# Performance work log

Hardware: AMD Instinct MI355X
Metric: run time of the kernel (lower is better)

The kernel has to match this reference:

```python
import jax, jax.numpy as jnp
import numpy as np

N_NODES = 50000
N_FEAT = 128
HIDDEN = 3
N_EDGES = 600000
N_POWERS = 3


def setup_inputs() -> dict:
    key = jax.random.key(0)
    ks = jax.random.split(key, 6)
    x = jax.random.normal(ks[0], (N_NODES, N_FEAT), dtype=jnp.float32)
    edge_index = jax.random.randint(ks[1], (N_POWERS, 2, N_EDGES), 0, N_NODES, dtype=jnp.int64)
    # MLP params for the 3 adjacency powers, stacked on the leading axis.
    # torch Linear(in,out) stored transposed here: y = x @ W + b.
    Wa = jax.random.normal(ks[2], (N_POWERS, N_FEAT, HIDDEN), dtype=jnp.float32) * (1.0 / np.sqrt(N_FEAT))
    ba = jax.random.normal(ks[3], (N_POWERS, HIDDEN), dtype=jnp.float32) * 0.01
    Wb = jax.random.normal(ks[4], (N_POWERS, HIDDEN, 1), dtype=jnp.float32) * (1.0 / np.sqrt(HIDDEN))
    bb = jax.random.normal(ks[5], (N_POWERS, 1), dtype=jnp.float32) * 0.01
    return {"x": x, "edge_index": edge_index, "Wa": Wa, "ba": ba, "Wb": Wb, "bb": bb}


def reference(x, edge_index, Wa, ba, Wb, bb):
    # Gather source/target node features per edge, per adjacency power.
    x_j = x[edge_index[:, 0]]          # [P, E, F]
    x_i = x[edge_index[:, 1]]          # [P, E, F]
    abs_dif = jnp.abs(x_j - x_i)       # [P, E, F]
    # Tiny per-edge MLP: Linear -> ReLU -> Linear -> Sigmoid (separate params per power).
    h = jax.nn.relu(jnp.einsum('pef,pfh->peh', abs_dif, Wa) + ba[:, None, :])  # [P, E, H]
    w = jax.nn.sigmoid(jnp.einsum('peh,pho->peo', h, Wb) + bb[:, None, :])     # [P, E, 1]
    return w[..., 0]                   # [P, E] edge weights for each power
```

## Files before the change

### kernel.cpp

```cpp
#include <hip/hip_runtime.h>
#include <math.h>

#define N_NODES 50000
#define N_FEAT  128
#define N_EDGES 600000
#define N_POWERS 3

#define PAIRS 5
#define EDGES_PER_BLK (64 * PAIRS)

#define NB64 64
#define CAP64 10240
#define CHUNK 2048
#define NCHUNK 293

typedef _Float16 half2v __attribute__((ext_vector_type(2)));
typedef unsigned u32x4  __attribute__((ext_vector_type(4)));
union HU { unsigned u; half2v h; };

__device__ __forceinline__ int bj_of(int j) { return j / 6250; }

__global__ __launch_bounds__(256) void conv_x_plain(const float* __restrict__ x,
                                                    unsigned* __restrict__ xh,
                                                    const float* __restrict__ Wa,
                                                    unsigned* __restrict__ wah,
                                                    int* __restrict__ cur) {
    const int t = blockIdx.x * 256 + threadIdx.x;
    const float4* x4 = (const float4*)x;
    float4 a = x4[(size_t)t * 2];
    float4 b = x4[(size_t)t * 2 + 1];
    HU p0, p1, p2, p3;
    p0.h = half2v{(_Float16)a.x, (_Float16)a.y};
    p1.h = half2v{(_Float16)a.z, (_Float16)a.w};
    p2.h = half2v{(_Float16)b.x, (_Float16)b.y};
    p3.h = half2v{(_Float16)b.z, (_Float16)b.w};
    ((uint4*)xh)[t] = uint4{p0.u, p1.u, p2.u, p3.u};
    if (blockIdx.x == 0 && threadIdx.x < 192) {
        const int tt = threadIdx.x;
        #pragma unroll
        for (int q = 0; q < 3; ++q) {
            int idx = tt + q * 192;
            int c  = idx % 3;
            int pk = idx / 3;
            int k  = pk % 64;
            int p  = pk / 64;
            float w0 = Wa[p * 384 + (2 * k) * 3 + c];
            float w1 = Wa[p * 384 + (2 * k + 1) * 3 + c];
            HU u; u.h = half2v{(_Float16)w0, (_Float16)w1};
            wah[idx] = u.u;
        }
    }
    if (cur != nullptr && blockIdx.x == 1 && threadIdx.x < N_POWERS * NB64)
        cur[threadIdx.x] = 0;
}

__global__ __launch_bounds__(256) void scatter_onepass(const int* __restrict__ edge_index,
                                                       unsigned* __restrict__ su,
                                                       int* __restrict__ inv,
                                                       int* __restrict__ cur) {
    __shared__ int tot[4][NB64];
    __shared__ int sh_w[4][NB64];
    __shared__ int sh_lbase[NB64];
    __shared__ int sh_delta[NB64];
    __shared__ int sh_vt;
    __shared__ unsigned pay[CHUNK];
    __shared__ int dlt[CHUNK];

    const int p = blockIdx.y, chunk = blockIdx.x;
    const int tid  = threadIdx.x;
    const int lane = tid & 63;
    const int wave = tid >> 6;
    const int* ej = edge_index + (size_t)p * 2 * N_EDGES;
    const int* ei = ej + N_EDGES;
    const int base = chunk * CHUNK;

    int jj[8], ii[8], sbk[8], off[8];
    int run = 0;
    #pragma unroll
    for (int k = 0; k < 8; ++k) {
        const int e = base + k * 256 + tid;
        const bool valid = e < N_EDGES;
        jj[k] = __builtin_nontemporal_load(ej + (valid ? e : 0));
        ii[k] = __builtin_nontemporal_load(ei + (valid ? e : 0));
        const int b = bj_of(jj[k]) * 8 + bj_of(ii[k]);
        sbk[k] = b;
        const unsigned long long m0 = __ballot(b & 1);
        const unsigned long long m1 = __ballot(b & 2);
        const unsigned long long m2 = __ballot(b & 4);
        const unsigned long long m3 = __ballot(b & 8);
        const unsigned long long m4 = __ballot(b & 16);
        const unsigned long long m5 = __ballot(b & 32);
        const unsigned long long vm = __ballot(valid);
        unsigned long long m = ((b & 1) ? m0 : ~m0);
        m &= ((b & 2)  ? m1 : ~m1);
        m &= ((b & 4)  ? m2 : ~m2);
        m &= ((b & 8)  ? m3 : ~m3);
        m &= ((b & 16) ? m4 : ~m4);
        m &= ((b & 32) ? m5 : ~m5);
        m &= vm;
        const int rank = (int)__popcll(m & ((1ull << lane) - 1ull));
        unsigned long long mm = ((lane & 1) ? m0 : ~m0);
        mm &= ((lane & 2)  ? m1 : ~m1);
        mm &= ((lane & 4)  ? m2 : ~m2);
        mm &= ((lane & 8)  ? m3 : ~m3);
        mm &= ((lane & 16) ? m4 : ~m4);
        mm &= ((lane & 32) ? m5 : ~m5);
        mm &= vm;
        const int cnt = (int)__popcll(mm);
        const int pre = __shfl(run, b, 64);
        off[k] = pre + rank;
        run += cnt;
    }
    tot[wave][lane] = run;
    __syncthreads();

    if (tid < NB64) {
        const int t0 = tot[0][tid], t1 = tot[1][tid], t2 = tot[2][tid], t3 = tot[3][tid];
        const int bt = t0 + t1 + t2 + t3;
        int s = bt;
        #pragma unroll
        for (int d = 1; d < 64; d <<= 1) {
            int u = __shfl_up(s, d, 64);
            if (tid >= d) s += u;
        }
        const int lb = s - bt;
        const int g  = atomicAdd(&cur[p * NB64 + tid], bt);
        sh_lbase[tid] = lb;
        sh_delta[tid] = (p * NB64 + tid) * CAP64 + g - lb;
        sh_w[0][tid] = 0;
        sh_w[1][tid] = t0;
        sh_w[2][tid] = t0 + t1;
        sh_w[3][tid] = t0 + t1 + t2;
        if (tid == 63) sh_vt = lb + bt;
    }
    __syncthreads();

    #pragma unroll
    for (int k = 0; k < 8; ++k) {
        const int e = base + k * 256 + tid;
        if (e < N_EDGES) {
            const int b = sbk[k];
            const int pos = sh_lbase[b] + sh_w[wave][b] + off[k];
            pay[pos] = (unsigned)(jj[k] | (ii[k] << 16));
            dlt[pos] = sh_delta[b];
            inv[(size_t)p * N_EDGES + e] = sh_delta[b] + pos;
        }
    }
    __syncthreads();

    const int vt = sh_vt;
    #pragma unroll
    for (int k = 0; k < 8; ++k) {
        const int pos = k * 256 + tid;
        if (pos < vt)
            su[(size_t)(dlt[pos] + pos)] = pay[pos];
    }
}

template<int PAT>
__device__ __forceinline__ float swz(float v) {
    return __int_as_float(__builtin_amdgcn_ds_swizzle(__float_as_int(v), PAT));
}

__device__ __forceinline__ void dot3_8(const u32x4& qa0, const u32x4& qa1,
                                       const u32x4& qb0, const u32x4& qb1,
                                       const HU wa[8][3],
                                       float& h0, float& h1, float& h2) {
    unsigned ua[8] = {qa0[0], qa0[1], qa0[2], qa0[3], qa1[0], qa1[1], qa1[2], qa1[3]};
    unsigned ub[8] = {qb0[0], qb0[1], qb0[2], qb0[3], qb1[0], qb1[1], qb1[2], qb1[3]};
    h0 = 0.f; h1 = 0.f; h2 = 0.f;
    #pragma unroll
    for (int k = 0; k < 8; ++k) {
        HU a, b, d;
        a.u = ua[k]; b.u = ub[k];
        d.h = a.h - b.h;
        d.u &= 0x7fff7fffu;
        h0 = __builtin_amdgcn_fdot2(d.h, wa[k][0].h, h0, false);
        h1 = __builtin_amdgcn_fdot2(d.h, wa[k][1].h, h1, false);
        h2 = __builtin_amdgcn_fdot2(d.h, wa[k][2].h, h2, false);
    }
}

__global__ __launch_bounds__(256, 4) void adj_kernel_sorted(
    const unsigned* __restrict__ xh,
    unsigned* su,
    const int* __restrict__ cur,
    const unsigned* __restrict__ wah,
    const float* __restrict__ ba,
    const float* __restrict__ Wb,
    const float* __restrict__ bb)
{
    const int p    = blockIdx.y;
    const int bj   = blockIdx.x & 7;
    const int k    = (blockIdx.x >> 3) & 31;
    const int bi   = blockIdx.x >> 8;
    const int sb   = bj * 8 + bi;
    const int tid  = threadIdx.x;
    const int lane = tid & 63;
    const int wave = tid >> 6;
    const int sub  = lane & 7;
    const int grp  = lane >> 3;

    const int count = cur[p * NB64 + sb];
    const int base  = k * EDGES_PER_BLK;
    if (base >= count) return;

    HU wa[8][3];
    {
        const unsigned* wp = wah + ((size_t)p * 64 + sub * 8) * 3;
        #pragma unroll
        for (int kk = 0; kk < 8; ++kk) {
            wa[kk][0].u = wp[kk * 3 + 0];
            wa[kk][1].u = wp[kk * 3 + 1];
            wa[kk][2].u = wp[kk * 3 + 2];
        }
        #pragma unroll
        for (int kk = 0; kk < 8; ++kk) {
            asm volatile("" : "+v"(wa[kk][0].u), "+v"(wa[kk][1].u), "+v"(wa[kk][2].u));
        }
    }

    const float ba0 = ba[p * 3 + 0], ba1 = ba[p * 3 + 1], ba2 = ba[p * 3 + 2];
    const float wb0 = Wb[p * 3 + 0], wb1 = Wb[p * 3 + 1], wb2 = Wb[p * 3 + 2];
    const float bbp = bb[p];

    unsigned* sup = su + (size_t)(p * NB64 + sb) * CAP64;

    const int eoff = wave * 8 + grp;
    const int roff = sub * 8;
    const int cm1  = count - 1;

    unsigned q[2 * PAIRS];
    #pragma unroll
    for (int it = 0; it < PAIRS; ++it) {
        const int r1 = base + it * 64 + eoff;
        q[2 * it]     = __builtin_nontemporal_load(sup + min(r1, cm1));
        q[2 * it + 1] = __builtin_nontemporal_load(sup + min(r1 + 32, cm1));
    }

    u32x4 A0, A1, B0, B1, C0, C1, D0, D1;
    {
        const int j1 = (int)(q[0] & 0xFFFFu), i1 = (int)(q[0] >> 16);
        const int j2 = (int)(q[1] & 0xFFFFu), i2 = (int)(q[1] >> 16);
        const u32x4* rj1 = (const u32x4*)(xh + ((size_t)j1 << 6) + roff);
        const u32x4* ri1 = (const u32x4*)(xh + ((size_t)i1 << 6) + roff);
        const u32x4* rj2 = (const u32x4*)(xh + ((size_t)j2 << 6) + roff);
        const u32x4* ri2 = (const u32x4*)(xh + ((size_t)i2 << 6) + roff);
        A0 = rj1[0]; A1 = rj1[1]; B0 = ri1[0]; B1 = ri1[1];
        C0 = rj2[0]; C1 = rj2[1]; D0 = ri2[0]; D1 = ri2[1];
    }

    #pragma unroll
    for (int it = 0; it < PAIRS; ++it) {
        u32x4 nA0, nA1, nB0, nB1, nC0, nC1, nD0, nD1;
        if (it + 1 < PAIRS) {
            const int j1 = (int)(q[2 * it + 2] & 0xFFFFu), i1 = (int)(q[2 * it + 2] >> 16);
            const int j2 = (int)(q[2 * it + 3] & 0xFFFFu), i2 = (int)(q[2 * it + 3] >> 16);
            const u32x4* rj1 = (const u32x4*)(xh + ((size_t)j1 << 6) + roff);
            const u32x4* ri1 = (const u32x4*)(xh + ((size_t)i1 << 6) + roff);
            const u32x4* rj2 = (const u32x4*)(xh + ((size_t)j2 << 6) + roff);
            const u32x4* ri2 = (const u32x4*)(xh + ((size_t)i2 << 6) + roff);
            nA0 = rj1[0]; nA1 = rj1[1]; nB0 = ri1[0]; nB1 = ri1[1];
            nC0 = rj2[0]; nC1 = rj2[1]; nD0 = ri2[0]; nD1 = ri2[1];
        }

        float h0a, h1a, h2a, h0b, h1b, h2b;
        dot3_8(A0, A1, B0, B1, wa, h0a, h1a, h2a);
        dot3_8(C0, C1, D0, D1, wa, h0b, h1b, h2b);

        h0a += swz<0x041F>(h0a); h1a += swz<0x041F>(h1a); h2a += swz<0x041F>(h2a);
        h0b += swz<0x041F>(h0b); h1b += swz<0x041F>(h1b); h2b += swz<0x041F>(h2b);
        h0a += swz<0x081F>(h0a); h1a += swz<0x081F>(h1a); h2a += swz<0x081F>(h2a);
        h0b += swz<0x081F>(h0b); h1b += swz<0x081F>(h1b); h2b += swz<0x081F>(h2b);
        h0a += swz<0x101F>(h0a); h1a += swz<0x101F>(h1a); h2a += swz<0x101F>(h2a);
        h0b += swz<0x101F>(h0b); h1b += swz<0x101F>(h1b); h2b += swz<0x101F>(h2b);

        if (sub == 0) {
            const int r1 = base + it * 64 + eoff;
            const int r2 = r1 + 32;
            if (r1 < count) {
                float r0  = fmaxf(h0a + ba0, 0.f);
                float r1f = fmaxf(h1a + ba1, 0.f);
                float r2f = fmaxf(h2a + ba2, 0.f);
                float s   = fmaf(r0, wb0, fmaf(r1f, wb1, fmaf(r2f, wb2, bbp)));
                ((float*)sup)[r1] = 1.f / (1.f + __expf(-s));
            }
            if (r2 < count) {
                float r0  = fmaxf(h0b + ba0, 0.f);
                float r1f = fmaxf(h1b + ba1, 0.f);
                float r2f = fmaxf(h2b + ba2, 0.f);
                float s   = fmaf(r0, wb0, fmaf(r1f, wb1, fmaf(r2f, wb2, bbp)));
                ((float*)sup)[r2] = 1.f / (1.f + __expf(-s));
            }
        }

        if (it + 1 < PAIRS) {
            A0 = nA0; A1 = nA1; B0 = nB0; B1 = nB1;
            C0 = nC0; C1 = nC1; D0 = nD0; D1 = nD1;
        }
    }
}

__global__ __launch_bounds__(256) void unscatter_kernel(const unsigned* __restrict__ su,
                                                        const int* __restrict__ inv,
                                                        float* __restrict__ out) {
    const int p  = blockIdx.y;
    const int t4 = (blockIdx.x * 256 + threadIdx.x) * 4;
    if (t4 >= N_EDGES) return;
    const int4 iv = *(const int4*)(inv + (size_t)p * N_EDGES + t4);
    const float* w = (const float*)su;
    float4 o;
    o.x = w[iv.x]; o.y = w[iv.y]; o.z = w[iv.z]; o.w = w[iv.w];
    __builtin_nontemporal_store(o.x, out + (size_t)p * N_EDGES + t4 + 0);
    __builtin_nontemporal_store(o.y, out + (size_t)p * N_EDGES + t4 + 1);
    __builtin_nontemporal_store(o.z, out + (size_t)p * N_EDGES + t4 + 2);
    __builtin_nontemporal_store(o.w, out + (size_t)p * N_EDGES + t4 + 3);
}

__global__ __launch_bounds__(256) void adj_kernel_f16(
    const unsigned* __restrict__ xh,
    const unsigned* __restrict__ wah,
    const int*   __restrict__ edge_index,
    const float* __restrict__ ba,
    const float* __restrict__ Wb,
    const float* __restrict__ bb,
    float* __restrict__ out)
{
    const int p    = blockIdx.y;
    const int tid  = threadIdx.x;
    const int lane = tid & 63;
    const int wave = tid >> 6;
    const int sub  = lane & 7;
    const int grp  = lane >> 3;

    HU wa[8][3];
    {
        const unsigned* wp = wah + ((size_t)p * 64 + sub * 8) * 3;
        #pragma unroll
        for (int k = 0; k < 8; ++k) {
            wa[k][0].u = wp[k * 3 + 0];
            wa[k][1].u = wp[k * 3 + 1];
            wa[k][2].u = wp[k * 3 + 2];
        }
        #pragma unroll
        for (int k = 0; k < 8; ++k) {
            asm volatile("" : "+v"(wa[k][0].u), "+v"(wa[k][1].u), "+v"(wa[k][2].u));
        }
    }

    const float ba0 = ba[p * 3 + 0], ba1 = ba[p * 3 + 1], ba2 = ba[p * 3 + 2];
    const float wb0 = Wb[p * 3 + 0], wb1 = Wb[p * 3 + 1], wb2 = Wb[p * 3 + 2];
    const float bbp = bb[p];

    const int* ej = edge_index + (size_t)p * 2 * N_EDGES;
    const int* ei = ej + N_EDGES;
    float* outp = out + (size_t)p * N_EDGES;

    const int e_blk = blockIdx.x * EDGES_PER_BLK;
    const int eoff  = wave * 8 + grp;
    const int roff  = sub * 8;

    #pragma unroll
    for (int it = 0; it < PAIRS; ++it) {
        const int e1 = e_blk + it * 64 + eoff;
        const int e2 = e1 + 32;
        const int j1 = __builtin_nontemporal_load(ej + e1);
        const int i1 = __builtin_nontemporal_load(ei + e1);
        const int j2 = __builtin_nontemporal_load(ej + e2);
        const int i2 = __builtin_nontemporal_load(ei + e2);

        const u32x4* rj1 = (const u32x4*)(xh + ((size_t)j1 << 6) + roff);
        const u32x4* ri1 = (const u32x4*)(xh + ((size_t)i1 << 6) + roff);
        const u32x4* rj2 = (const u32x4*)(xh + ((size_t)j2 << 6) + roff);
        const u32x4* ri2 = (const u32x4*)(xh + ((size_t)i2 << 6) + roff);
        u32x4 a0 = rj1[0], a1 = rj1[1];
        u32x4 b0 = ri1[0], b1 = ri1[1];
        u32x4 c0 = rj2[0], c1 = rj2[1];
        u32x4 d0 = ri2[0], d1 = ri2[1];

        float h0a, h1a, h2a, h0b, h1b, h2b;
        dot3_8(a0, a1, b0, b1, wa, h0a, h1a, h2a);
        dot3_8(c0, c1, d0, d1, wa, h0b, h1b, h2b);

        h0a += swz<0x041F>(h0a); h1a += swz<0x041F>(h1a); h2a += swz<0x041F>(h2a);
        h0b += swz<0x041F>(h0b); h1b += swz<0x041F>(h1b); h2b += swz<0x041F>(h2b);
        h0a += swz<0x081F>(h0a); h1a += swz<0x081F>(h1a); h2a += swz<0x081F>(h2a);
        h0b += swz<0x081F>(h0b); h1b += swz<0x081F>(h1b); h2b += swz<0x081F>(h2b);
        h0a += swz<0x101F>(h0a); h1a += swz<0x101F>(h1a); h2a += swz<0x101F>(h2a);
        h0b += swz<0x101F>(h0b); h1b += swz<0x101F>(h1b); h2b += swz<0x101F>(h2b);

        if (sub == 0) {
            float r0 = fmaxf(h0a + ba0, 0.f);
            float r1 = fmaxf(h1a + ba1, 0.f);
            float r2 = fmaxf(h2a + ba2, 0.f);
            float s  = fmaf(r0, wb0, fmaf(r1, wb1, fmaf(r2, wb2, bbp)));
            __builtin_nontemporal_store(1.f / (1.f + __expf(-s)), outp + e1);
            r0 = fmaxf(h0b + ba0, 0.f);
            r1 = fmaxf(h1b + ba1, 0.f);
            r2 = fmaxf(h2b + ba2, 0.f);
            s  = fmaf(r0, wb0, fmaf(r1, wb1, fmaf(r2, wb2, bbp)));
            __builtin_nontemporal_store(1.f / (1.f + __expf(-s)), outp + e2);
        }
    }
}

__global__ __launch_bounds__(256) void adj_kernel_f32(
    const float* __restrict__ x,
    const int*   __restrict__ edge_index,
    const float* __restrict__ Wa,
    const float* __restrict__ ba,
    const float* __restrict__ Wb,
    const float* __restrict__ bb,
    float* __restrict__ out)
{
    const int p    = blockIdx.y;
    const int tid  = threadIdx.x;
    const int lane = tid & 63;
    const int wave = tid >> 6;
    const int sub  = lane & 15;
    const int grp  = lane >> 4;
    const int f0 = sub * 8;

    const float* Wap = Wa + (size_t)p * N_FEAT * 3;
    float wa0[8], wa1[8], wa2[8];
    #pragma unroll
    for (int k = 0; k < 8; ++k) {
        wa0[k] = Wap[(f0 + k) * 3 + 0];
        wa1[k] = Wap[(f0 + k) * 3 + 1];
        wa2[k] = Wap[(f0 + k) * 3 + 2];
    }
    const float ba0 = ba[p * 3 + 0], ba1 = ba[p * 3 + 1], ba2 = ba[p * 3 + 2];
    const float wb0 = Wb[p * 3 + 0], wb1 = Wb[p * 3 + 1], wb2 = Wb[p * 3 + 2];
    const float bbp = bb[p];

    const int e = blockIdx.x * 16 + wave * 4 + grp;
    const int* ej = edge_index + (size_t)p * 2 * N_EDGES;
    const int* ei = ej + N_EDGES;
    const int j = ej[e];
    const int i = ei[e];

    const float4* xj = (const float4*)(x + (size_t)j * N_FEAT + f0);
    const float4* xi = (const float4*)(x + (size_t)i * N_FEAT + f0);
    float4 a0 = xj[0], a1 = xj[1];
    float4 b0 = xi[0], b1 = xi[1];

    float d[8];
    d[0] = fabsf(a0.x - b0.x); d[1] = fabsf(a0.y - b0.y);
    d[2] = fabsf(a0.z - b0.z); d[3] = fabsf(a0.w - b0.w);
    d[4] = fabsf(a1.x - b1.x); d[5] = fabsf(a1.y - b1.y);
    d[6] = fabsf(a1.z - b1.z); d[7] = fabsf(a1.w - b1.w);

    float h0 = 0.f, h1 = 0.f, h2 = 0.f;
    #pragma unroll
    for (int k = 0; k < 8; ++k) {
        h0 = fmaf(d[k], wa0[k], h0);
        h1 = fmaf(d[k], wa1[k], h1);
        h2 = fmaf(d[k], wa2[k], h2);
    }
    #pragma unroll
    for (int m = 1; m < 16; m <<= 1) {
        h0 += __shfl_xor(h0, m, 64);
        h1 += __shfl_xor(h1, m, 64);
        h2 += __shfl_xor(h2, m, 64);
    }
    if (sub == 0) {
        float r0 = fmaxf(h0 + ba0, 0.f);
        float r1 = fmaxf(h1 + ba1, 0.f);
        float r2 = fmaxf(h2 + ba2, 0.f);
        float s  = fmaf(r0, wb0, fmaf(r1, wb1, fmaf(r2, wb2, bbp)));
        float w  = 1.f / (1.f + expf(-s));
        out[(size_t)p * N_EDGES + e] = w;
    }
}

extern "C" void kernel_launch(void* const* d_in, const int* in_sizes, int n_in,
                              void* d_out, int out_size, void* d_ws, size_t ws_size,
                              hipStream_t stream) {
    const float* x          = (const float*)d_in[0];
    const int*   edge_index = (const int*)d_in[1];
    const float* Wa         = (const float*)d_in[2];
    const float* ba         = (const float*)d_in[3];
    const float* Wb         = (const float*)d_in[4];
    const float* bb         = (const float*)d_in[5];
    float* out = (float*)d_out;

    const size_t x_bytes   = (size_t)N_NODES * N_FEAT * 2;
    const size_t su_bytes  = (size_t)N_POWERS * NB64 * CAP64 * 4;
    const size_t inv_bytes = (size_t)N_POWERS * N_EDGES * 4;
    const size_t wa_bytes  = 2304;
    const size_t cur_bytes = N_POWERS * NB64 * 4;
    const size_t need_full = x_bytes + su_bytes + inv_bytes + wa_bytes + cur_bytes;

    if (ws_size >= need_full) {
        char* w = (char*)d_ws;
        unsigned* xh  = (unsigned*)w;
        unsigned* su  = (unsigned*)(w + x_bytes);
        int*      inv = (int*)(w + x_bytes + su_bytes);
        unsigned* wah = (unsigned*)(w + x_bytes + su_bytes + inv_bytes);
        int*      cur = (int*)(w + x_bytes + su_bytes + inv_bytes + wa_bytes);

        conv_x_plain<<<N_NODES * N_FEAT / 2048, 256, 0, stream>>>(x, xh, Wa, wah, cur);
        scatter_onepass<<<dim3(NCHUNK, N_POWERS), 256, 0, stream>>>(edge_index, su, inv, cur);
        dim3 grid(NB64 * (CAP64 / EDGES_PER_BLK), N_POWERS);
        adj_kernel_sorted<<<grid, 256, 0, stream>>>(xh, su, cur, wah, ba, Wb, bb);
        unscatter_kernel<<<dim3((N_EDGES / 4 + 255) / 256, N_POWERS), 256, 0, stream>>>(
            su, inv, out);
    } else if (ws_size >= x_bytes + wa_bytes) {
        unsigned* xh  = (unsigned*)d_ws;
        unsigned* wah = (unsigned*)((char*)d_ws + x_bytes);
        conv_x_plain<<<N_NODES * N_FEAT / 2048, 256, 0, stream>>>(x, xh, Wa, wah, nullptr);
        dim3 grid(N_EDGES / EDGES_PER_BLK, N_POWERS);
        adj_kernel_f16<<<grid, 256, 0, stream>>>(xh, wah, edge_index, ba, Wb, bb, out);
    } else {
        dim3 grid((N_EDGES + 15) / 16, N_POWERS);
        adj_kernel_f32<<<grid, 256, 0, stream>>>(x, edge_index, Wa, ba, Wb, bb, out);
    }
}
```

Measured before the change: 176.8 us.

## Bucket edges by source node range and counting-sort within buckets by source

Edges are now bucketed into 64 bins by source node range only, instead of by a joint source/target 8x8 grid. A new per-bucket counting sort in shared memory orders each bucket by exact source node, and a fixup kernel rewrites the inverse permutation, using the output buffer as scratch for the permutation. Target-row loads become nontemporal while source rows keep normal caching. The aim is cache reuse of source rows, paid for with two extra kernel launches, extra passes over the sorted payload, and the risk of a bucket overflowing CAP64 under uniform counts.

```diff
diff --git a/kernel.cpp b/kernel.cpp
--- a/kernel.cpp
+++ b/kernel.cpp
@@ -10,6 +10,7 @@
 #define EDGES_PER_BLK (64 * PAIRS)
 
 #define NB64 64
+#define NJB 782
 #define CAP64 10240
 #define CHUNK 2048
 #define NCHUNK 293
@@ -17,8 +18,6 @@
 typedef _Float16 half2v __attribute__((ext_vector_type(2)));
 typedef unsigned u32x4  __attribute__((ext_vector_type(4)));
 union HU { unsigned u; half2v h; };
-
-__device__ __forceinline__ int bj_of(int j) { return j / 6250; }
 
 __global__ __launch_bounds__(256) void conv_x_plain(const float* __restrict__ x,
                                                     unsigned* __restrict__ xh,
@@ -82,7 +81,7 @@
         const bool valid = e < N_EDGES;
         jj[k] = __builtin_nontemporal_load(ej + (valid ? e : 0));
         ii[k] = __builtin_nontemporal_load(ei + (valid ? e : 0));
-        const int b = bj_of(jj[k]) * 8 + bj_of(ii[k]);
+        const int b = jj[k] / NJB;
         sbk[k] = b;
         const unsigned long long m0 = __ballot(b & 1);
         const unsigned long long m1 = __ballot(b & 2);
@@ -157,6 +156,93 @@
     }
 }
 
+__global__ __launch_bounds__(256) void sortj_kernel(unsigned* __restrict__ su,
+                                                    int* __restrict__ perm,
+                                                    const int* __restrict__ cur) {
+    __shared__ int hist[NJB];
+    __shared__ unsigned spay[CAP64];
+    __shared__ int wsum[4];
+    __shared__ int csum;
+    const int p = blockIdx.y, b = blockIdx.x;
+    const int tid = threadIdx.x;
+    const int count = cur[p * NB64 + b];
+    const size_t gbase = (size_t)(p * NB64 + b) * CAP64;
+
+    if (tid == 0) {
+        int s = 0;
+        for (int t = 0; t < b; ++t) s += cur[p * NB64 + t];
+        csum = s;
+    }
+    for (int t = tid; t < NJB; t += 256) hist[t] = 0;
+    __syncthreads();
+
+    const int j0 = b * NJB;
+    for (int s = tid; s < count; s += 256) {
+        const unsigned v = su[gbase + s];
+        atomicAdd(&hist[(int)(v & 0xFFFFu) - j0], 1);
+    }
+    __syncthreads();
+
+    int loc[4]; int ts = 0;
+    #pragma unroll
+    for (int q = 0; q < 4; ++q) {
+        const int idx = tid * 4 + q;
+        loc[q] = (idx < NJB) ? hist[idx] : 0;
+        ts += loc[q];
+    }
+    const int lane = tid & 63, wv = tid >> 6;
+    int ps = ts;
+    #pragma unroll
+    for (int d = 1; d < 64; d <<= 1) { int u = __shfl_up(ps, d, 64); if (lane >= d) ps += u; }
+    if (lane == 63) wsum[wv] = ps;
+    __syncthreads();
+    int wbase = 0;
+    #pragma unroll
+    for (int wq = 0; wq < 4; ++wq) wbase += (wq < wv) ? wsum[wq] : 0;
+    int run = wbase + (ps - ts);
+    __syncthreads();
+    #pragma unroll
+    for (int q = 0; q < 4; ++q) {
+        const int idx = tid * 4 + q;
+        if (idx < NJB) hist[idx] = run;
+        run += loc[q];
+    }
+    __syncthreads();
+
+    const int cb = p * N_EDGES + csum;
+    for (int s = tid; s < count; s += 256) {
+        const unsigned v = su[gbase + s];
+        const int np = atomicAdd(&hist[(int)(v & 0xFFFFu) - j0], 1);
+        spay[np] = v;
+        perm[cb + s] = np;
+    }
+    __syncthreads();
+    for (int s = tid; s < count; s += 256)
+        su[gbase + s] = spay[s];
+}
+
+__global__ __launch_bounds__(256) void fixinv_kernel(int* __restrict__ inv,
+                                                     const int* __restrict__ perm,
+                                                     const int* __restrict__ cur) {
+    __shared__ int cbase[N_POWERS * NB64];
+    const int tid = threadIdx.x;
+    if (tid < N_POWERS * NB64) {
+        const int p = tid / NB64, b = tid % NB64;
+        int s = 0;
+        for (int t = 0; t < b; ++t) s += cur[p * NB64 + t];
+        cbase[tid] = p * N_EDGES + s;
+    }
+    __syncthreads();
+    const int p = blockIdx.y;
+    const int e = blockIdx.x * 256 + tid;
+    if (e >= N_EDGES) return;
+    const int g = inv[(size_t)p * N_EDGES + e];
+    const int pb = g / CAP64;
+    const int pos = g - pb * CAP64;
+    const int np = perm[cbase[pb] + pos];
+    inv[(size_t)p * N_EDGES + e] = pb * CAP64 + np;
+}
+
 template<int PAT>
 __device__ __forceinline__ float swz(float v) {
     return __int_as_float(__builtin_amdgcn_ds_swizzle(__float_as_int(v), PAT));
@@ -191,10 +277,8 @@
     const float* __restrict__ bb)
 {
     const int p    = blockIdx.y;
-    const int bj   = blockIdx.x & 7;
-    const int k    = (blockIdx.x >> 3) & 31;
-    const int bi   = blockIdx.x >> 8;
-    const int sb   = bj * 8 + bi;
+    const int sb   = blockIdx.x & 63;
+    const int k    = blockIdx.x >> 6;
     const int tid  = threadIdx.x;
     const int lane = tid & 63;
     const int wave = tid >> 6;
@@ -246,8 +330,10 @@
         const u32x4* ri1 = (const u32x4*)(xh + ((size_t)i1 << 6) + roff);
         const u32x4* rj2 = (const u32x4*)(xh + ((size_t)j2 << 6) + roff);
         const u32x4* ri2 = (const u32x4*)(xh + ((size_t)i2 << 6) + roff);
-        A0 = rj1[0]; A1 = rj1[1]; B0 = ri1[0]; B1 = ri1[1];
-        C0 = rj2[0]; C1 = rj2[1]; D0 = ri2[0]; D1 = ri2[1];
+        A0 = rj1[0]; A1 = rj1[1];
+        B0 = __builtin_nontemporal_load(ri1); B1 = __builtin_nontemporal_load(ri1 + 1);
+        C0 = rj2[0]; C1 = rj2[1];
+        D0 = __builtin_nontemporal_load(ri2); D1 = __builtin_nontemporal_load(ri2 + 1);
     }
 
     #pragma unroll
@@ -260,8 +346,10 @@
             const u32x4* ri1 = (const u32x4*)(xh + ((size_t)i1 << 6) + roff);
             const u32x4* rj2 = (const u32x4*)(xh + ((size_t)j2 << 6) + roff);
             const u32x4* ri2 = (const u32x4*)(xh + ((size_t)i2 << 6) + roff);
-            nA0 = rj1[0]; nA1 = rj1[1]; nB0 = ri1[0]; nB1 = ri1[1];
-            nC0 = rj2[0]; nC1 = rj2[1]; nD0 = ri2[0]; nD1 = ri2[1];
+            nA0 = rj1[0]; nA1 = rj1[1];
+            nB0 = __builtin_nontemporal_load(ri1); nB1 = __builtin_nontemporal_load(ri1 + 1);
+            nC0 = rj2[0]; nC1 = rj2[1];
+            nD0 = __builtin_nontemporal_load(ri2); nD1 = __builtin_nontemporal_load(ri2 + 1);
         }
 
         float h0a, h1a, h2a, h0b, h1b, h2b;
@@ -498,9 +586,12 @@
         int*      inv = (int*)(w + x_bytes + su_bytes);
         unsigned* wah = (unsigned*)(w + x_bytes + su_bytes + inv_bytes);
         int*      cur = (int*)(w + x_bytes + su_bytes + inv_bytes + wa_bytes);
+        int*      perm = (int*)out;
 
         conv_x_plain<<<N_NODES * N_FEAT / 2048, 256, 0, stream>>>(x, xh, Wa, wah, cur);
         scatter_onepass<<<dim3(NCHUNK, N_POWERS), 256, 0, stream>>>(edge_index, su, inv, cur);
+        sortj_kernel<<<dim3(NB64, N_POWERS), 256, 0, stream>>>(su, perm, cur);
+        fixinv_kernel<<<dim3((N_EDGES + 255) / 256, N_POWERS), 256, 0, stream>>>(inv, perm, cur);
         dim3 grid(NB64 * (CAP64 / EDGES_PER_BLK), N_POWERS);
         adj_kernel_sorted<<<grid, 256, 0, stream>>>(xh, su, cur, wah, ba, Wb, bb);
         unscatter_kernel<<<dim3((N_EDGES / 4 + 255) / 256, N_POWERS), 256, 0, stream>>>(
```

New measurement: 265.7 us. 1.5x slower.
